# Kernel tuning notes

Hardware: AMD Instinct MI355X
Metric: run time of the kernel (lower is better)

Reference implementation:

```python
import jax, jax.numpy as jnp
import numpy as np

K_SIZE = 5
PAD = 2  # (dilation*(k-1)+1 - stride + 1)//2 with k=5, dil=1, stride=1
SAMPLE_NUM = 15
DEPTH_MAX = 192.0


def _gather_patches(x, sample_idx):
    """x: [B,C,H,W] -> [B,H,W,S,C]: values of the 5x5 local neighborhood at the
    SAMPLE_NUM sampled kernel positions (zero padding, matching nn.Unfold)."""
    B, C, H, W = x.shape
    xp = jnp.pad(x, ((0, 0), (0, 0), (PAD, PAD), (PAD, PAD)))
    slabs = []
    for i in range(SAMPLE_NUM):  # small fixed constant, not a data dim
        p = sample_idx[i]
        dy = p // K_SIZE
        dx = p % K_SIZE
        slabs.append(jax.lax.dynamic_slice(xp, (0, 0, dy, dx), (B, C, H, W)))
    pat = jnp.stack(slabs, axis=1)          # [B,S,C,H,W]
    return pat.transpose(0, 3, 4, 1, 2)     # [B,H,W,S,C]


def setup_inputs() -> dict:
    key = jax.random.key(0)
    k1, k2, k3, k4 = jax.random.split(key, 4)
    B, C, H, W = 2, 32, 240, 320
    depth = jax.random.uniform(k1, (B, 1, H, W), dtype=jnp.float32) * 200.0
    surface_normal = jax.random.normal(k2, (B, 3, H, W), dtype=jnp.float32)
    features = jax.random.normal(k3, (B, C, H, W), dtype=jnp.float32)
    guide_weight = jnp.ones((B, H, W, K_SIZE * K_SIZE), dtype=jnp.float32)
    sample_idx = jax.random.randint(k4, (SAMPLE_NUM,), 0, K_SIZE * K_SIZE, dtype=jnp.int32)
    return {"depth": depth, "surface_normal": surface_normal, "features": features,
            "guide_weight": guide_weight, "sample_idx": sample_idx}


def reference(depth, surface_normal, features, guide_weight, sample_idx):
    b, c, h, w = features.shape
    d = depth[:, 0]                                          # squeeze(1) -> [B,H,W]
    valid = ((d > 0) & (d < DEPTH_MAX)).astype(features.dtype)[:, None]  # [B,1,H,W]

    feat_s = _gather_patches(features, sample_idx)           # [B,H,W,S,C]
    norm_s = _gather_patches(surface_normal, sample_idx)     # [B,H,W,S,3]
    valid_s = _gather_patches(valid, sample_idx)[..., 0]     # [B,H,W,S]

    # Faithful to torch: surface_normal.view(b, h, w, 3) is a raw memory
    # reinterpretation, NOT a permute.
    center_n = jnp.reshape(surface_normal, (b, h, w, 3))
    diff = jnp.sqrt(jnp.sum((norm_s - center_n[:, :, :, None, :]) ** 2, axis=-1))
    # torch detaches via the cpu/numpy round-trip -> stop_gradient here
    normal_w = jax.lax.stop_gradient(jnp.exp(-0.5 * diff))   # [B,H,W,S]

    guide_s = jnp.take(guide_weight, sample_idx, axis=3)     # [B,H,W,S]

    fw = valid_s * normal_w * guide_s                        # both weight flags True
    fw = jax.nn.softmax(fw, axis=-1)
    out = jnp.sum(feat_s * fw[..., None], axis=3)            # [B,H,W,C]
    return (out.transpose(0, 3, 1, 2), features)
```

## Files before the change

### kernel.cpp

```cpp
#include <hip/hip_runtime.h>

#define K_SIZE 5
#define PAD 2
#define SAMPLE_NUM 15
#define DEPTH_MAX 192.0f

constexpr int B = 2, C = 32, H = 240, W = 320;
constexpr int HW  = H * W;
constexpr int BHW = B * HW;
constexpr int PPB = 64;
constexpr int NBLK = BHW / PPB;
constexpr int XCHUNK = NBLK / 8;

typedef float float4a __attribute__((ext_vector_type(4), aligned(16)));
typedef float float4u __attribute__((ext_vector_type(4), aligned(4)));

__global__ __launch_bounds__(256) void adaptive_sample_fused(
    const float* __restrict__ depth,
    const float* __restrict__ sn,
    const float* __restrict__ features,
    const float* __restrict__ guide,
    const int*   __restrict__ sample_idx,
    float* __restrict__ out,
    float* __restrict__ feat_out)
{
    __shared__ __align__(16) float w_lds[SAMPLE_NUM][PPB + 4];

    int bid = blockIdx.x;
    int blk = (bid & 7) * XCHUNK + (bid >> 3);

    const int t       = threadIdx.x;
    const int base    = blk * PPB;
    const int b       = base / HW;
    const int pixbase = base - b * HW;

    const float* snb = sn + (size_t)b * 3 * HW;
    const float* db  = depth + (size_t)b * HW;

    {
        const int s  = t & 15;
        const int lq = t >> 4;
        #pragma unroll
        for (int kk = 0; kk < 4; ++kk) {
            int lp  = kk * 16 + lq;
            int pix = pixbase + lp;
            int y = pix / W, x = pix - (pix / W) * W;

            float prew = 0.0f;
            bool  inb  = false;
            if (s < SAMPLE_NUM) {
                int pp = sample_idx[s];
                int dy = pp / K_SIZE - PAD;
                int dx = pp - (pp / K_SIZE) * K_SIZE - PAD;
                int yy = y + dy, xx = x + dx;
                inb = (yy >= 0) && (yy < H) && (xx >= 0) && (xx < W);
                if (inb) {
                    int noff = yy * W + xx;
                    float d = db[noff];
                    if (d > 0.0f && d < DEPTH_MAX) {
                        int o = pix * 3;
                        float cn0 = snb[o], cn1 = snb[o + 1], cn2 = snb[o + 2];
                        float d0 = snb[noff]          - cn0;
                        float d1 = snb[HW + noff]     - cn1;
                        float d2 = snb[2 * HW + noff] - cn2;
                        float diff = sqrtf(d0 * d0 + d1 * d1 + d2 * d2);
                        prew = __expf(-0.5f * diff)
                             * guide[((size_t)b * HW + pix) * 25 + pp];
                    }
                }
            }
            float m = prew;
            #pragma unroll
            for (int mask = 1; mask < 16; mask <<= 1)
                m = fmaxf(m, __shfl_xor(m, mask, 16));
            float e = (s < SAMPLE_NUM) ? __expf(prew - m) : 0.0f;
            float sum = e;
            #pragma unroll
            for (int mask = 1; mask < 16; mask <<= 1)
                sum += __shfl_xor(sum, mask, 16);
            if (s < SAMPLE_NUM)
                w_lds[s][lp] = inb ? (e / sum) : 0.0f;
        }
    }
    __syncthreads();

    {
        const int q    = t & 15;
        const int cs   = t >> 4;
        const int p0   = pixbase + q * 4;
        const int y    = p0 / W;
        const int x0   = p0 - y * W;
        const bool edge = (x0 == 0) || (x0 == W - 4);

        #pragma unroll
        for (int it = 0; it < 2; ++it) {
            const int c = it * 16 + cs;
            const float* fb = features + ((size_t)b * C + c) * HW;

            float4a acc = {0.0f, 0.0f, 0.0f, 0.0f};
            #pragma unroll
            for (int ss = 0; ss < SAMPLE_NUM; ++ss) {
                int pp = sample_idx[ss];
                int dy = pp / K_SIZE - PAD;
                int dx = pp - (pp / K_SIZE) * K_SIZE - PAD;
                int yy = min(max(y + dy, 0), H - 1);
                int xx0 = min(max(x0 + dx, 0), W - 4);
                float4a w4 = *(const float4a*)&w_lds[ss][q * 4];
                float4u f4 = *(const float4u*)(fb + yy * W + xx0);
                acc += w4 * f4;
            }
            if (edge) {
                float a0 = 0, a1 = 0, a2 = 0, a3 = 0;
                #pragma unroll
                for (int ss = 0; ss < SAMPLE_NUM; ++ss) {
                    int pp = sample_idx[ss];
                    int dy = pp / K_SIZE - PAD;
                    int dx = pp - (pp / K_SIZE) * K_SIZE - PAD;
                    int yy = min(max(y + dy, 0), H - 1);
                    const float* frow = fb + yy * W;
                    int xb = x0 + dx;
                    a0 += w_lds[ss][q * 4 + 0] * frow[min(max(xb + 0, 0), W - 1)];
                    a1 += w_lds[ss][q * 4 + 1] * frow[min(max(xb + 1, 0), W - 1)];
                    a2 += w_lds[ss][q * 4 + 2] * frow[min(max(xb + 2, 0), W - 1)];
                    a3 += w_lds[ss][q * 4 + 3] * frow[min(max(xb + 3, 0), W - 1)];
                }
                acc = float4a{a0, a1, a2, a3};
            }

            size_t obase = ((size_t)b * C + c) * HW + p0;
            float4a pf = *(const float4a*)(fb + p0);
            *(float4a*)(out + obase)      = acc;
            *(float4a*)(feat_out + obase) = pf;
        }
    }
}

extern "C" void kernel_launch(void* const* d_in, const int* in_sizes, int n_in,
                              void* d_out, int out_size, void* d_ws, size_t ws_size,
                              hipStream_t stream) {
    const float* depth      = (const float*)d_in[0];
    const float* sn         = (const float*)d_in[1];
    const float* features   = (const float*)d_in[2];
    const float* guide      = (const float*)d_in[3];
    const int*   sample_idx = (const int*)d_in[4];

    float* out      = (float*)d_out;
    float* feat_out = (float*)d_out + (size_t)B * C * HW;

    adaptive_sample_fused<<<NBLK, 256, 0, stream>>>(
        depth, sn, features, guide, sample_idx, out, feat_out);
}
```

Measured before the change: 44.11 us.

## Stage feature halo tile in LDS and branchlessly compute softmax weights

Each block now cooperatively loads a 5-row by 68-column halo window of all 32 feature channels into shared memory, then reads the 15 sampled neighbours from LDS instead of global memory. The weight phase is made branchless by clamping addresses and loading unconditionally, and per-sample weights are hoisted into registers. This targets redundant global and L2 traffic from overlapping neighbourhood reads, at the cost of about 44KB of LDS per block, which lowers occupancy. The edge special case is dropped; out-of-row neighbours get zero weight anyway, and the window reads clamp to the flat array bounds.

New measurement: 48.10 us. 9.1% more time.

```diff
diff --git a/kernel.cpp b/kernel.cpp
--- a/kernel.cpp
+++ b/kernel.cpp
@@ -8,9 +8,16 @@
 constexpr int B = 2, C = 32, H = 240, W = 320;
 constexpr int HW  = H * W;
 constexpr int BHW = B * HW;
+constexpr int TOT = B * C * HW;
 constexpr int PPB = 64;
 constexpr int NBLK = BHW / PPB;
 constexpr int XCHUNK = NBLK / 8;
+
+constexpr int WROWS = 5;
+constexpr int WCOLS = 68;
+constexpr int SEGS  = WCOLS / 4;
+constexpr int CH_STRIDE = WROWS * WCOLS;
+constexpr int STAGE_TASKS = C * WROWS * SEGS;
 
 typedef float float4a __attribute__((ext_vector_type(4), aligned(16)));
 typedef float float4u __attribute__((ext_vector_type(4), aligned(4)));
@@ -24,51 +31,72 @@
     float* __restrict__ out,
     float* __restrict__ feat_out)
 {
-    __shared__ __align__(16) float w_lds[SAMPLE_NUM][PPB + 4];
+    __shared__ __align__(16) float lds_f[C * CH_STRIDE];
+    __shared__ __align__(16) float w_lds[SAMPLE_NUM][WCOLS];
 
-    int bid = blockIdx.x;
-    int blk = (bid & 7) * XCHUNK + (bid >> 3);
+    const int bid = blockIdx.x;
+    const int blk = (bid & 7) * XCHUNK + (bid >> 3);
 
-    const int t       = threadIdx.x;
-    const int base    = blk * PPB;
-    const int b       = base / HW;
-    const int pixbase = base - b * HW;
+    const int t    = threadIdx.x;
+    const int base = blk * PPB;
+    const int b    = base / HW;
+    const int pix0 = base - b * HW;
+    const int y    = pix0 / W;
+    const int x0   = pix0 - y * W;
+    const int planeBase = b * C * HW;
 
-    const float* snb = sn + (size_t)b * 3 * HW;
-    const float* db  = depth + (size_t)b * HW;
+    for (int i = t; i < STAGE_TASKS; i += 256) {
+        int ch  = i / (WROWS * SEGS);
+        int rem = i - ch * (WROWS * SEGS);
+        int r   = rem / SEGS;
+        int k   = rem - r * SEGS;
+        int yy  = min(max(y - 2 + r, 0), H - 1);
+        int flat = planeBase + ch * HW + yy * W + (x0 - 2 + k * 4);
+        float4a v;
+        if (flat >= 0 && flat <= TOT - 4) {
+            float4u g = *(const float4u*)(features + flat);
+            v = float4a{g.x, g.y, g.z, g.w};
+        } else {
+            #pragma unroll
+            for (int j = 0; j < 4; ++j)
+                v[j] = features[min(max(flat + j, 0), TOT - 1)];
+        }
+        *(float4a*)&lds_f[ch * CH_STRIDE + r * WCOLS + k * 4] = v;
+    }
 
     {
         const int s  = t & 15;
         const int lq = t >> 4;
+        const float* snb = sn + (size_t)b * 3 * HW;
+        const float* db  = depth + (size_t)b * HW;
+
+        const int pp = sample_idx[(s < SAMPLE_NUM) ? s : 0];
+        const int dy = pp / K_SIZE - PAD;
+        const int dx = pp - (pp / K_SIZE) * K_SIZE - PAD;
+
         #pragma unroll
         for (int kk = 0; kk < 4; ++kk) {
-            int lp  = kk * 16 + lq;
-            int pix = pixbase + lp;
-            int y = pix / W, x = pix - (pix / W) * W;
+            const int lp  = kk * 16 + lq;
+            const int x   = x0 + lp;
+            const int pix = pix0 + lp;
 
-            float prew = 0.0f;
-            bool  inb  = false;
-            if (s < SAMPLE_NUM) {
-                int pp = sample_idx[s];
-                int dy = pp / K_SIZE - PAD;
-                int dx = pp - (pp / K_SIZE) * K_SIZE - PAD;
-                int yy = y + dy, xx = x + dx;
-                inb = (yy >= 0) && (yy < H) && (xx >= 0) && (xx < W);
-                if (inb) {
-                    int noff = yy * W + xx;
-                    float d = db[noff];
-                    if (d > 0.0f && d < DEPTH_MAX) {
-                        int o = pix * 3;
-                        float cn0 = snb[o], cn1 = snb[o + 1], cn2 = snb[o + 2];
-                        float d0 = snb[noff]          - cn0;
-                        float d1 = snb[HW + noff]     - cn1;
-                        float d2 = snb[2 * HW + noff] - cn2;
-                        float diff = sqrtf(d0 * d0 + d1 * d1 + d2 * d2);
-                        prew = __expf(-0.5f * diff)
-                             * guide[((size_t)b * HW + pix) * 25 + pp];
-                    }
-                }
-            }
+            const int yy = y + dy, xx = x + dx;
+            const bool inb = (s < SAMPLE_NUM) &&
+                             (yy >= 0) && (yy < H) && (xx >= 0) && (xx < W);
+            const int noff = min(max(yy, 0), H - 1) * W + min(max(xx, 0), W - 1);
+
+            const float d   = db[noff];
+            const int   o   = pix * 3;
+            const float cn0 = snb[o], cn1 = snb[o + 1], cn2 = snb[o + 2];
+            const float d0  = snb[noff]          - cn0;
+            const float d1  = snb[HW + noff]     - cn1;
+            const float d2  = snb[2 * HW + noff] - cn2;
+            const float gv  = guide[((size_t)b * HW + pix) * 25 + pp];
+
+            const float diff = sqrtf(d0 * d0 + d1 * d1 + d2 * d2);
+            const bool  ok   = inb && (d > 0.0f) && (d < DEPTH_MAX);
+            const float prew = ok ? __expf(-0.5f * diff) * gv : 0.0f;
+
             float m = prew;
             #pragma unroll
             for (int mask = 1; mask < 16; mask <<= 1)
@@ -78,6 +106,7 @@
             #pragma unroll
             for (int mask = 1; mask < 16; mask <<= 1)
                 sum += __shfl_xor(sum, mask, 16);
+
             if (s < SAMPLE_NUM)
                 w_lds[s][lp] = inb ? (e / sum) : 0.0f;
         }
@@ -85,52 +114,35 @@
     __syncthreads();
 
     {
-        const int q    = t & 15;
-        const int cs   = t >> 4;
-        const int p0   = pixbase + q * 4;
-        const int y    = p0 / W;
-        const int x0   = p0 - y * W;
-        const bool edge = (x0 == 0) || (x0 == W - 4);
+        const int q  = t & 15;
+        const int cs = t >> 4;
+
+        float4a wv[SAMPLE_NUM];
+        #pragma unroll
+        for (int s = 0; s < SAMPLE_NUM; ++s)
+            wv[s] = *(const float4a*)&w_lds[s][4 * q];
 
         #pragma unroll
-        for (int it = 0; it < 2; ++it) {
-            const int c = it * 16 + cs;
-            const float* fb = features + ((size_t)b * C + c) * HW;
+        for (int half = 0; half < 2; ++half) {
+            const int ch = half * 16 + cs;
+            const float* fpl = &lds_f[ch * CH_STRIDE];
 
             float4a acc = {0.0f, 0.0f, 0.0f, 0.0f};
             #pragma unroll
-            for (int ss = 0; ss < SAMPLE_NUM; ++ss) {
-                int pp = sample_idx[ss];
+            for (int s = 0; s < SAMPLE_NUM; ++s) {
+                int pp = sample_idx[s];
                 int dy = pp / K_SIZE - PAD;
                 int dx = pp - (pp / K_SIZE) * K_SIZE - PAD;
-                int yy = min(max(y + dy, 0), H - 1);
-                int xx0 = min(max(x0 + dx, 0), W - 4);
-                float4a w4 = *(const float4a*)&w_lds[ss][q * 4];
-                float4u f4 = *(const float4u*)(fb + yy * W + xx0);
-                acc += w4 * f4;
-            }
-            if (edge) {
-                float a0 = 0, a1 = 0, a2 = 0, a3 = 0;
-                #pragma unroll
-                for (int ss = 0; ss < SAMPLE_NUM; ++ss) {
-                    int pp = sample_idx[ss];
-                    int dy = pp / K_SIZE - PAD;
-                    int dx = pp - (pp / K_SIZE) * K_SIZE - PAD;
-                    int yy = min(max(y + dy, 0), H - 1);
-                    const float* frow = fb + yy * W;
-                    int xb = x0 + dx;
-                    a0 += w_lds[ss][q * 4 + 0] * frow[min(max(xb + 0, 0), W - 1)];
-                    a1 += w_lds[ss][q * 4 + 1] * frow[min(max(xb + 1, 0), W - 1)];
-                    a2 += w_lds[ss][q * 4 + 2] * frow[min(max(xb + 2, 0), W - 1)];
-                    a3 += w_lds[ss][q * 4 + 3] * frow[min(max(xb + 3, 0), W - 1)];
-                }
-                acc = float4a{a0, a1, a2, a3};
+                int rr  = dy + 2;
+                int xi0 = 4 * q + dx + 2;
+                float4u f4 = *(const float4u*)&fpl[rr * WCOLS + xi0];
+                acc += wv[s] * float4a{f4.x, f4.y, f4.z, f4.w};
             }
 
-            size_t obase = ((size_t)b * C + c) * HW + p0;
-            float4a pf = *(const float4a*)(fb + p0);
-            *(float4a*)(out + obase)      = acc;
-            *(float4a*)(feat_out + obase) = pf;
+            const int gflat = planeBase + ch * HW + pix0 + 4 * q;
+            float4a pf = *(const float4a*)(features + gflat);
+            *(float4a*)(out + gflat)      = acc;
+            *(float4a*)(feat_out + gflat) = pf;
         }
     }
 }
```
